# Kernel optimization log

Measured on AMD Instinct MI355X. Metric: run time of the kernel, lower is better.

Reference implementation:

```python
import jax, jax.numpy as jnp
import numpy as np


def setup_inputs() -> dict:
    key = jax.random.key(0)
    k1, k2, k3 = jax.random.split(key, 3)
    B, H, G, L, S, D = 2, 8, 4, 2048, 2048, 128
    q = jax.random.normal(k1, (B, H, G, L, D), dtype=jnp.float32)
    k = jax.random.normal(k2, (B, H, 1, S, D), dtype=jnp.float32)
    v = jax.random.normal(k3, (B, H, 1, S, D), dtype=jnp.float32)
    return {"q": q, "k": k, "v": v}


def reference(q, k, v):
    # q: [B,H,G,L,D]; k,v: [B,H,1,S,D] broadcast over G groups.
    # NOTE: original module does NOT scale by 1/sqrt(D).
    kk = jnp.squeeze(k, axis=2)  # [B,H,S,D]
    vv = jnp.squeeze(v, axis=2)  # [B,H,S,D]
    scores = jnp.einsum('bhgld,bhsd->bhgls', q, kk)  # [B,H,G,L,S]
    probs = jax.nn.softmax(scores, axis=-1)
    return jnp.einsum('bhgls,bhsd->bhgld', probs, vv)  # [B,H,G,L,D]
```

## Files before the change

kernel.cpp:

```cpp
#include <hip/hip_runtime.h>
#include <hip/hip_bf16.h>
#include <math.h>

typedef __bf16 bf16x8 __attribute__((ext_vector_type(8)));
typedef __bf16 bf16x4 __attribute__((ext_vector_type(4)));
typedef float  f32x4  __attribute__((ext_vector_type(4)));

constexpr int D   = 128;
constexpr int LQ  = 2048;
constexpr int SK  = 2048;
constexpr int BM  = 256;
constexpr int BN  = 64;
constexpr int NKV = 16;
constexpr int NT  = SK / BN;

__device__ __forceinline__ void load_lds16(const void* g, void* l) {
  __builtin_amdgcn_global_load_lds((const __attribute__((address_space(1))) unsigned*)g,
                                   (__attribute__((address_space(3))) unsigned*)l, 16, 0, 0);
}

__global__ __launch_bounds__(256) void conv_k(const float* __restrict__ k,
                                              __bf16* __restrict__ khi,
                                              __bf16* __restrict__ klo) {
  const size_t i = ((size_t)blockIdx.x * 256 + threadIdx.x) * 4;
  f32x4 a = *(const f32x4*)(k + i);
  bf16x4 hi, lo;
#pragma unroll
  for (int j = 0; j < 4; ++j) {
    hi[j] = (__bf16)a[j];
    lo[j] = (__bf16)(a[j] - (float)hi[j]);
  }
  *(bf16x4*)(khi + i) = hi;
  *(bf16x4*)(klo + i) = lo;
}

__global__ __launch_bounds__(256) void transpose_v(const float* __restrict__ v,
                                                   __bf16* __restrict__ vt) {
  const int b    = blockIdx.x;
  const int bh   = b >> 6;
  const int t2   = (b & 63) * 256 + threadIdx.x;
  const int d    = t2 & 127;
  const int slot = t2 >> 7;
  const int G    = slot >> 1;
  const int h2   = slot & 1;
  const float* src = v + ((size_t)bh * SK + 32 * G) * D + d;
  bf16x8 o0, o1;
#pragma unroll
  for (int qq = 0; qq < 2; ++qq)
#pragma unroll
    for (int h = 0; h < 2; ++h)
#pragma unroll
      for (int r = 0; r < 4; ++r) {
        const int idx = 8 * qq + 4 * h + r;
        const int w   = 16 * h + 4 * (2 * h2 + qq) + r;
        const __bf16 val = (__bf16)src[(size_t)w * D];
        if (idx < 8) o0[idx] = val; else o1[idx - 8] = val;
      }
  __bf16* dst = vt + ((size_t)bh * D + d) * SK + 32 * G + 16 * h2;
  *(bf16x8*)dst = o0;
  *(bf16x8*)(dst + 8) = o1;
}

__global__ __launch_bounds__(512, 2)
void gqa_fwd(const float* __restrict__ qg, const __bf16* __restrict__ khi_g,
             const __bf16* __restrict__ klo_g, const __bf16* __restrict__ vt_g,
             float* __restrict__ outg)
{
  __shared__ alignas(16) __bf16 Kh[2][BN * D];
  __shared__ alignas(16) __bf16 Kl[2][BN * D];
  __shared__ alignas(16) __bf16 Vs[2][D * BN];

  const int bid   = blockIdx.x;
  const int xcd   = bid & 7;
  const int idx   = bid >> 3;
  const int bh    = 2 * xcd + (idx & 1);
  const int grp   = (idx >> 1) & 3;
  const int qtile = idx >> 3;
  const int bhg   = bh * 4 + grp;

  const int tid  = threadIdx.x;
  const int wave = tid >> 6;
  const int lane = tid & 63;
  const int i16  = lane & 15;
  const int quad = lane >> 4;

  const float*  qbase = qg + (size_t)bhg * (LQ * D) + (size_t)(qtile * BM) * D;
  const __bf16* khb   = khi_g + (size_t)bh * (SK * D);
  const __bf16* klb   = klo_g + (size_t)bh * (SK * D);
  const __bf16* vtb   = vt_g + (size_t)bh * (D * SK);

  auto stage = [&](int s0, int buf) {
#pragma unroll
    for (int c = 0; c < 2; ++c) {
      const int wc   = 2 * wave + c;
      const int srow = wc * 4 + (lane >> 4);
      const int jk   = (lane & 15) ^ (srow & 15);
      load_lds16(khb + (size_t)(s0 + srow) * D + 8 * jk, (char*)&Kh[buf][0] + wc * 1024);
      load_lds16(klb + (size_t)(s0 + srow) * D + 8 * jk, (char*)&Kl[buf][0] + wc * 1024);
      const int drow = wc * 8 + (lane >> 3);
      const int jv   = (lane & 7) ^ (drow & 7);
      load_lds16(vtb + (size_t)drow * SK + s0 + 8 * jv, (char*)&Vs[buf][0] + wc * 1024);
    }
  };

  stage(0, 0);

  constexpr float LOG2E = 1.44269504089f;
  bf16x8 qhi[2][4], qlo[2][4];
#pragma unroll
  for (int u = 0; u < 2; ++u) {
    const float* qp = qbase + (size_t)(32 * wave + 16 * u + i16) * D + 8 * quad;
#pragma unroll
    for (int t = 0; t < 4; ++t) {
      f32x4 a = *(const f32x4*)(qp + 32 * t);
      f32x4 b = *(const f32x4*)(qp + 32 * t + 4);
#pragma unroll
      for (int j = 0; j < 4; ++j) {
        const float a2 = a[j] * LOG2E;
        const float b2 = b[j] * LOG2E;
        qhi[u][t][j]     = (__bf16)a2;
        qlo[u][t][j]     = (__bf16)(a2 - (float)qhi[u][t][j]);
        qhi[u][t][j + 4] = (__bf16)b2;
        qlo[u][t][j + 4] = (__bf16)(b2 - (float)qhi[u][t][j + 4]);
      }
    }
  }

  f32x4 o_acc[2][8];
#pragma unroll
  for (int u = 0; u < 2; ++u)
#pragma unroll
    for (int c = 0; c < 8; ++c) o_acc[u][c] = (f32x4){0.f, 0.f, 0.f, 0.f};
  float m_r[2] = {-INFINITY, -INFINITY};
  float l_r[2] = {0.f, 0.f};

  asm volatile("s_waitcnt vmcnt(0)" ::: "memory");
  __syncthreads();

  for (int it = 0; it < NT; ++it) {
    const int cur = it & 1;
    const __bf16* khc = &Kh[cur][0];
    const __bf16* klc = &Kl[cur][0];
    const __bf16* vsc = &Vs[cur][0];

    if (it + 1 < NT) stage((it + 1) * BN, cur ^ 1);

    f32x4 sf[2][4];
#pragma unroll
    for (int u = 0; u < 2; ++u)
#pragma unroll
      for (int n = 0; n < 4; ++n) sf[u][n] = (f32x4){0.f, 0.f, 0.f, 0.f};
    __builtin_amdgcn_s_setprio(1);
#pragma unroll
    for (int n = 0; n < 4; ++n) {
#pragma unroll
      for (int t = 0; t < 4; ++t) {
        const int ke = (16 * n + i16) * 128 + 8 * ((4 * t + quad) ^ i16);
        bf16x8 kh = *(const bf16x8*)&khc[ke];
        bf16x8 kl = *(const bf16x8*)&klc[ke];
#pragma unroll
        for (int u = 0; u < 2; ++u) {
          sf[u][n] = __builtin_amdgcn_mfma_f32_16x16x32_bf16(kh, qhi[u][t], sf[u][n], 0, 0, 0);
          sf[u][n] = __builtin_amdgcn_mfma_f32_16x16x32_bf16(kh, qlo[u][t], sf[u][n], 0, 0, 0);
          sf[u][n] = __builtin_amdgcn_mfma_f32_16x16x32_bf16(kl, qhi[u][t], sf[u][n], 0, 0, 0);
        }
      }
    }
    __builtin_amdgcn_s_setprio(0);

    bf16x8 pb[2][2];
#pragma unroll
    for (int u = 0; u < 2; ++u) {
      const float ma = fmaxf(fmaxf(sf[u][0][0], sf[u][0][1]), fmaxf(sf[u][0][2], sf[u][0][3]));
      const float mb = fmaxf(fmaxf(sf[u][1][0], sf[u][1][1]), fmaxf(sf[u][1][2], sf[u][1][3]));
      const float mc = fmaxf(fmaxf(sf[u][2][0], sf[u][2][1]), fmaxf(sf[u][2][2], sf[u][2][3]));
      const float md = fmaxf(fmaxf(sf[u][3][0], sf[u][3][1]), fmaxf(sf[u][3][2], sf[u][3][3]));
      float mx = fmaxf(fmaxf(ma, mb), fmaxf(mc, md));
      mx = fmaxf(mx, __shfl_xor(mx, 16, 64));
      mx = fmaxf(mx, __shfl_xor(mx, 32, 64));
      if (__any(mx > m_r[u] + 11.5f)) {
        const float mnew  = fmaxf(m_r[u], mx);
        const float alpha = exp2f(m_r[u] - mnew);
        m_r[u] = mnew;
        l_r[u] *= alpha;
#pragma unroll
        for (int c = 0; c < 8; ++c) o_acc[u][c] = o_acc[u][c] * alpha;
      }
      f32x4 rs4 = (f32x4){0.f, 0.f, 0.f, 0.f};
#pragma unroll
      for (int t = 0; t < 2; ++t)
#pragma unroll
        for (int h = 0; h < 2; ++h)
#pragma unroll
          for (int r = 0; r < 4; ++r) {
            const float p   = exp2f(sf[u][2 * t + h][r] - m_r[u]);
            const __bf16 pv = (__bf16)p;
            pb[u][t][4 * h + r] = pv;
            rs4[r] += (float)pv;
          }
      float rs = (rs4[0] + rs4[1]) + (rs4[2] + rs4[3]);
      rs += __shfl_xor(rs, 16, 64);
      rs += __shfl_xor(rs, 32, 64);
      l_r[u] += rs;
    }

    __builtin_amdgcn_s_setprio(1);
#pragma unroll
    for (int c = 0; c < 8; ++c) {
      const int row = 16 * c + i16;
#pragma unroll
      for (int t = 0; t < 2; ++t) {
        bf16x8 av = *(const bf16x8*)&vsc[row * 64 + 8 * ((4 * t + quad) ^ (i16 & 7))];
#pragma unroll
        for (int u = 0; u < 2; ++u)
          o_acc[u][c] = __builtin_amdgcn_mfma_f32_16x16x32_bf16(av, pb[u][t], o_acc[u][c], 0, 0, 0);
      }
    }
    __builtin_amdgcn_s_setprio(0);

    asm volatile("s_waitcnt vmcnt(0)" ::: "memory");
    __syncthreads();
  }

  float* obase = outg + (size_t)bhg * (LQ * D) + (size_t)(qtile * BM) * D;
#pragma unroll
  for (int u = 0; u < 2; ++u) {
    const float inv = 1.f / l_r[u];
    float* op = obase + (size_t)(32 * wave + 16 * u + i16) * D;
#pragma unroll
    for (int c = 0; c < 8; ++c) {
      f32x4 r4 = o_acc[u][c] * inv;
      *(f32x4*)(op + 16 * c + 4 * quad) = r4;
    }
  }
}

extern "C" void kernel_launch(void* const* d_in, const int* in_sizes, int n_in,
                              void* d_out, int out_size, void* d_ws, size_t ws_size,
                              hipStream_t stream) {
  const float* q = (const float*)d_in[0];
  const float* k = (const float*)d_in[1];
  const float* v = (const float*)d_in[2];
  float* out = (float*)d_out;
  (void)in_sizes; (void)n_in; (void)out_size; (void)ws_size;

  const size_t kv_elems = (size_t)NKV * SK * D;
  __bf16* khi = (__bf16*)d_ws;
  __bf16* klo = khi + kv_elems;
  __bf16* vt  = klo + kv_elems;

  conv_k<<<dim3(kv_elems / (256 * 4)), 256, 0, stream>>>(k, khi, klo);
  transpose_v<<<dim3(NKV * 64), 256, 0, stream>>>(v, vt);
  gqa_fwd<<<dim3(8 * (LQ / BM) * 8), 512, 0, stream>>>(q, khi, klo, vt, out);
}
```

Measured before the change: 414.1 us.

## Split per-iteration work into two row-halves to interleave softmax with MFMA

Restructures the inner loop so that each 16-row half runs QK, softmax and PV in sequence, instead of batching both halves per phase. This lets the softmax VALU work of one half overlap with the MFMAs of the other. It also drops the conditional lazy rescale and always rescales, drops the setprio hints, and issues the next-tile prefetch unconditionally with a wrapped index. K fragments are reloaded from LDS twice and V fragments twice, adding LDS traffic; the unconditional rescale also adds VALU work.

```diff
diff --git a/kernel.cpp b/kernel.cpp
--- a/kernel.cpp
+++ b/kernel.cpp
@@ -17,6 +17,13 @@
 __device__ __forceinline__ void load_lds16(const void* g, void* l) {
   __builtin_amdgcn_global_load_lds((const __attribute__((address_space(1))) unsigned*)g,
                                    (__attribute__((address_space(3))) unsigned*)l, 16, 0, 0);
+}
+
+__device__ __forceinline__ f32x4 vmax4(f32x4 a, f32x4 b) {
+  f32x4 r;
+  r[0] = fmaxf(a[0], b[0]); r[1] = fmaxf(a[1], b[1]);
+  r[2] = fmaxf(a[2], b[2]); r[3] = fmaxf(a[3], b[3]);
+  return r;
 }
 
 __global__ __launch_bounds__(256) void conv_k(const float* __restrict__ k,
@@ -143,14 +150,11 @@
     const __bf16* klc = &Kl[cur][0];
     const __bf16* vsc = &Vs[cur][0];
 
-    if (it + 1 < NT) stage((it + 1) * BN, cur ^ 1);
-
-    f32x4 sf[2][4];
-#pragma unroll
-    for (int u = 0; u < 2; ++u)
-#pragma unroll
-      for (int n = 0; n < 4; ++n) sf[u][n] = (f32x4){0.f, 0.f, 0.f, 0.f};
-    __builtin_amdgcn_s_setprio(1);
+    stage(((it + 1) & (NT - 1)) * BN, cur ^ 1);
+
+    f32x4 s0[4], s1[4];
+#pragma unroll
+    for (int n = 0; n < 4; ++n) s0[n] = (f32x4){0.f, 0.f, 0.f, 0.f};
 #pragma unroll
     for (int n = 0; n < 4; ++n) {
 #pragma unroll
@@ -158,34 +162,36 @@
         const int ke = (16 * n + i16) * 128 + 8 * ((4 * t + quad) ^ i16);
         bf16x8 kh = *(const bf16x8*)&khc[ke];
         bf16x8 kl = *(const bf16x8*)&klc[ke];
-#pragma unroll
-        for (int u = 0; u < 2; ++u) {
-          sf[u][n] = __builtin_amdgcn_mfma_f32_16x16x32_bf16(kh, qhi[u][t], sf[u][n], 0, 0, 0);
-          sf[u][n] = __builtin_amdgcn_mfma_f32_16x16x32_bf16(kh, qlo[u][t], sf[u][n], 0, 0, 0);
-          sf[u][n] = __builtin_amdgcn_mfma_f32_16x16x32_bf16(kl, qhi[u][t], sf[u][n], 0, 0, 0);
-        }
-      }
-    }
-    __builtin_amdgcn_s_setprio(0);
-
-    bf16x8 pb[2][2];
-#pragma unroll
-    for (int u = 0; u < 2; ++u) {
-      const float ma = fmaxf(fmaxf(sf[u][0][0], sf[u][0][1]), fmaxf(sf[u][0][2], sf[u][0][3]));
-      const float mb = fmaxf(fmaxf(sf[u][1][0], sf[u][1][1]), fmaxf(sf[u][1][2], sf[u][1][3]));
-      const float mc = fmaxf(fmaxf(sf[u][2][0], sf[u][2][1]), fmaxf(sf[u][2][2], sf[u][2][3]));
-      const float md = fmaxf(fmaxf(sf[u][3][0], sf[u][3][1]), fmaxf(sf[u][3][2], sf[u][3][3]));
-      float mx = fmaxf(fmaxf(ma, mb), fmaxf(mc, md));
+        s0[n] = __builtin_amdgcn_mfma_f32_16x16x32_bf16(kh, qhi[0][t], s0[n], 0, 0, 0);
+        s0[n] = __builtin_amdgcn_mfma_f32_16x16x32_bf16(kh, qlo[0][t], s0[n], 0, 0, 0);
+        s0[n] = __builtin_amdgcn_mfma_f32_16x16x32_bf16(kl, qhi[0][t], s0[n], 0, 0, 0);
+      }
+    }
+
+#pragma unroll
+    for (int n = 0; n < 4; ++n) s1[n] = (f32x4){0.f, 0.f, 0.f, 0.f};
+#pragma unroll
+    for (int n = 0; n < 4; ++n) {
+#pragma unroll
+      for (int t = 0; t < 4; ++t) {
+        const int ke = (16 * n + i16) * 128 + 8 * ((4 * t + quad) ^ i16);
+        bf16x8 kh = *(const bf16x8*)&khc[ke];
+        bf16x8 kl = *(const bf16x8*)&klc[ke];
+        s1[n] = __builtin_amdgcn_mfma_f32_16x16x32_bf16(kh, qhi[1][t], s1[n], 0, 0, 0);
+        s1[n] = __builtin_amdgcn_mfma_f32_16x16x32_bf16(kh, qlo[1][t], s1[n], 0, 0, 0);
+        s1[n] = __builtin_amdgcn_mfma_f32_16x16x32_bf16(kl, qhi[1][t], s1[n], 0, 0, 0);
+      }
+    }
+
+    bf16x8 pb0[2], pb1[2];
+    {
+      f32x4 vm = vmax4(vmax4(s0[0], s0[1]), vmax4(s0[2], s0[3]));
+      float mx = fmaxf(fmaxf(vm[0], vm[1]), fmaxf(vm[2], vm[3]));
       mx = fmaxf(mx, __shfl_xor(mx, 16, 64));
       mx = fmaxf(mx, __shfl_xor(mx, 32, 64));
-      if (__any(mx > m_r[u] + 11.5f)) {
-        const float mnew  = fmaxf(m_r[u], mx);
-        const float alpha = exp2f(m_r[u] - mnew);
-        m_r[u] = mnew;
-        l_r[u] *= alpha;
-#pragma unroll
-        for (int c = 0; c < 8; ++c) o_acc[u][c] = o_acc[u][c] * alpha;
-      }
+      const float mnew  = fmaxf(m_r[0], mx);
+      const float alpha = exp2f(m_r[0] - mnew);
+      m_r[0] = mnew;
       f32x4 rs4 = (f32x4){0.f, 0.f, 0.f, 0.f};
 #pragma unroll
       for (int t = 0; t < 2; ++t)
@@ -193,30 +199,66 @@
         for (int h = 0; h < 2; ++h)
 #pragma unroll
           for (int r = 0; r < 4; ++r) {
-            const float p   = exp2f(sf[u][2 * t + h][r] - m_r[u]);
+            const float p   = exp2f(s0[2 * t + h][r] - mnew);
             const __bf16 pv = (__bf16)p;
-            pb[u][t][4 * h + r] = pv;
+            pb0[t][4 * h + r] = pv;
             rs4[r] += (float)pv;
           }
       float rs = (rs4[0] + rs4[1]) + (rs4[2] + rs4[3]);
       rs += __shfl_xor(rs, 16, 64);
       rs += __shfl_xor(rs, 32, 64);
-      l_r[u] += rs;
-    }
-
-    __builtin_amdgcn_s_setprio(1);
+      l_r[0] = l_r[0] * alpha + rs;
+#pragma unroll
+      for (int c = 0; c < 8; ++c) o_acc[0][c] = o_acc[0][c] * alpha;
+    }
+
 #pragma unroll
     for (int c = 0; c < 8; ++c) {
       const int row = 16 * c + i16;
 #pragma unroll
       for (int t = 0; t < 2; ++t) {
         bf16x8 av = *(const bf16x8*)&vsc[row * 64 + 8 * ((4 * t + quad) ^ (i16 & 7))];
-#pragma unroll
-        for (int u = 0; u < 2; ++u)
-          o_acc[u][c] = __builtin_amdgcn_mfma_f32_16x16x32_bf16(av, pb[u][t], o_acc[u][c], 0, 0, 0);
-      }
-    }
-    __builtin_amdgcn_s_setprio(0);
+        o_acc[0][c] = __builtin_amdgcn_mfma_f32_16x16x32_bf16(av, pb0[t], o_acc[0][c], 0, 0, 0);
+      }
+    }
+
+    {
+      f32x4 vm = vmax4(vmax4(s1[0], s1[1]), vmax4(s1[2], s1[3]));
+      float mx = fmaxf(fmaxf(vm[0], vm[1]), fmaxf(vm[2], vm[3]));
+      mx = fmaxf(mx, __shfl_xor(mx, 16, 64));
+      mx = fmaxf(mx, __shfl_xor(mx, 32, 64));
+      const float mnew  = fmaxf(m_r[1], mx);
+      const float alpha = exp2f(m_r[1] - mnew);
+      m_r[1] = mnew;
+      f32x4 rs4 = (f32x4){0.f, 0.f, 0.f, 0.f};
+#pragma unroll
+      for (int t = 0; t < 2; ++t)
+#pragma unroll
+        for (int h = 0; h < 2; ++h)
+#pragma unroll
+          for (int r = 0; r < 4; ++r) {
+            const float p   = exp2f(s1[2 * t + h][r] - mnew);
+            const __bf16 pv = (__bf16)p;
+            pb1[t][4 * h + r] = pv;
+            rs4[r] += (float)pv;
+          }
+      float rs = (rs4[0] + rs4[1]) + (rs4[2] + rs4[3]);
+      rs += __shfl_xor(rs, 16, 64);
+      rs += __shfl_xor(rs, 32, 64);
+      l_r[1] = l_r[1] * alpha + rs;
+#pragma unroll
+      for (int c = 0; c < 8; ++c) o_acc[1][c] = o_acc[1][c] * alpha;
+    }
+
+#pragma unroll
+    for (int c = 0; c < 8; ++c) {
+      const int row = 16 * c + i16;
+#pragma unroll
+      for (int t = 0; t < 2; ++t) {
+        bf16x8 av = *(const bf16x8*)&vsc[row * 64 + 8 * ((4 * t + quad) ^ (i16 & 7))];
+        o_acc[1][c] = __builtin_amdgcn_mfma_f32_16x16x32_bf16(av, pb1[t], o_acc[1][c], 0, 0, 0);
+      }
+    }
 
     asm volatile("s_waitcnt vmcnt(0)" ::: "memory");
     __syncthreads();
```

Result: slower. 428.7 us (+3.5%).
